# Performance work log

Measured on AMD Instinct MI355X. Metric: run time of the kernel, lower is better.

## Reference

```python
import jax, jax.numpy as jnp
import numpy as np

N_LEFT, N_RIGHT, E = 5000, 20000, 400000
HID, EDIM, NH, HD = 128, 4, 8, 16


def setup_inputs() -> dict:
    key = jax.random.key(0)
    ks = jax.random.split(key, 16)
    def lin(k, fi, fo):
        return jax.random.normal(k, (fi, fo), jnp.float32) / np.sqrt(fi)
    inp = {
        'left': jax.random.normal(ks[0], (N_LEFT, HID), jnp.float32),
        'right': jax.random.normal(ks[1], (N_RIGHT, HID), jnp.float32),
        'edge_features': jax.random.normal(ks[2], (E, EDIM), jnp.float32),
        'edge_src': jax.random.randint(ks[3], (E,), 0, N_LEFT, jnp.int32),
        'edge_dst': jax.random.randint(ks[4], (E,), 0, N_RIGHT, jnp.int32),
        'Wq': lin(ks[5], HID, HID),
        'Wk': lin(ks[6], HID, HID),
        'Wv': lin(ks[7], HID, HID),
        'Wke': lin(ks[8], EDIM, HID),
        'Wve': lin(ks[9], EDIM, HID),
        'Wout': lin(ks[10], HID, HID),
        'bn_gamma': jnp.ones((HID,), jnp.float32),
        'bn_beta': jnp.zeros((HID,), jnp.float32),
        'W1': lin(ks[11], 2 * HID, HID),
        'b1': jnp.zeros((HID,), jnp.float32),
        'W2': lin(ks[12], HID, HID),
        'b2': jnp.zeros((HID,), jnp.float32),
    }
    return inp


def _bipartite_attn(left, right, edge_features, edge_src, edge_dst,
                    Wq, Wk, Wv, Wke, Wve, Wout, bn_gamma, bn_beta, W1, b1, W2, b2):
    nr = right.shape[0]
    # project nodes once, then gather per edge (same math as gather-then-project)
    q = (right @ Wq).reshape(nr, NH, HD)[edge_dst]          # [E, H, D]
    k = (left @ Wk).reshape(-1, NH, HD)[edge_src]           # [E, H, D]
    v = (left @ Wv).reshape(-1, NH, HD)[edge_src]           # [E, H, D]
    ke = (edge_features @ Wke).reshape(-1, NH, HD)          # [E, H, D]
    ve = (edge_features @ Wve).reshape(-1, NH, HD)          # [E, H, D]
    logits = jnp.sum(q * (k + ke), axis=-1) / np.sqrt(HD)   # [E, H]
    # segment softmax over destination nodes (pyg_softmax)
    seg_max = jax.ops.segment_max(logits, edge_dst, num_segments=nr)  # [NR, H]
    seg_max = jnp.where(jnp.isfinite(seg_max), seg_max, 0.0)
    ex = jnp.exp(logits - seg_max[edge_dst])
    seg_sum = jax.ops.segment_sum(ex, edge_dst, num_segments=nr)      # [NR, H]
    alpha = ex / (seg_sum[edge_dst] + 1e-16)                          # [E, H]
    msg = (v + ve) * alpha[..., None]                                  # [E, H, D]
    agg = jax.ops.segment_sum(msg, edge_dst, num_segments=nr)         # [NR, H, D]
    out = agg.reshape(nr, NH * HD) @ Wout                              # [NR, HID]
    # BatchNorm1d (training-mode batch statistics, eps=1e-5)
    mean = jnp.mean(out, axis=0)
    var = jnp.var(out, axis=0)
    out = bn_gamma * (out - mean) * jax.lax.rsqrt(var + 1e-5) + bn_beta
    # output MLP on [out, right]
    h = jnp.concatenate([out, right], axis=-1) @ W1 + b1
    h = jax.nn.relu(h)
    return h @ W2 + b2


def reference(left, right, edge_features, edge_src, edge_dst,
              Wq, Wk, Wv, Wke, Wve, Wout, bn_gamma, bn_beta, W1, b1, W2, b2):
    return _bipartite_attn(left, right, edge_features, edge_src, edge_dst,
                           Wq, Wk, Wv, Wke, Wve, Wout, bn_gamma, bn_beta, W1, b1, W2, b2)
```

## Files before the change

kernel.cpp:

```cpp
#include <hip/hip_runtime.h>
#include <math.h>

#define N_LEFTC  5000
#define N_RIGHTC 20000
#define NEDGE    400000
#define MAXD     56

typedef __attribute__((ext_vector_type(8))) short bf16x8;
typedef __attribute__((ext_vector_type(4))) float f32x4;
typedef __attribute__((ext_vector_type(4))) unsigned short u16x4;
typedef __attribute__((ext_vector_type(8))) unsigned short u16x8;

__device__ __forceinline__ unsigned short f2bf(float x) {
    unsigned int u = __float_as_uint(x);
    u = (u + 0x7fffu + ((u >> 16) & 1u)) >> 16;
    return (unsigned short)u;
}
__device__ __forceinline__ float bf2f(unsigned short u) {
    return __uint_as_float(((unsigned int)u) << 16);
}

__device__ __forceinline__ bf16x8 loadA_f32(const float* p) {
    float4 f0 = *(const float4*)p;
    float4 f1 = *(const float4*)(p + 4);
    bf16x8 a;
    a[0] = (short)f2bf(f0.x); a[1] = (short)f2bf(f0.y);
    a[2] = (short)f2bf(f0.z); a[3] = (short)f2bf(f0.w);
    a[4] = (short)f2bf(f1.x); a[5] = (short)f2bf(f1.y);
    a[6] = (short)f2bf(f1.z); a[7] = (short)f2bf(f1.w);
    return a;
}

template<bool ABF, bool OBF>
__device__ __forceinline__ void gemm_body(const void* __restrict__ Av,
    const unsigned short* __restrict__ Bp, void* __restrict__ Cv, int M,
    int bid, int tid)
{
    const int l  = tid & 63;
    const int w  = tid >> 6;
    const int r0 = bid * 64 + w * 16;
    const int arow = r0 + (l & 15);
    const int kl = (l >> 4) * 8;
    f32x4 acc[8];
    #pragma unroll
    for (int ct = 0; ct < 8; ++ct) acc[ct] = (f32x4){0.f, 0.f, 0.f, 0.f};
    const bool aok = (arow < M);
    #pragma unroll
    for (int ks = 0; ks < 4; ++ks) {
        bf16x8 a = {0, 0, 0, 0, 0, 0, 0, 0};
        if (aok) {
            if (ABF) a = *(const bf16x8*)((const unsigned short*)Av + (size_t)arow * 128 + ks * 32 + kl);
            else     a = loadA_f32((const float*)Av + (size_t)arow * 128 + ks * 32 + kl);
        }
        #pragma unroll
        for (int ct = 0; ct < 8; ++ct) {
            bf16x8 b = *(const bf16x8*)(Bp + (((ks * 8 + ct) * 64 + l) << 3));
            acc[ct] = __builtin_amdgcn_mfma_f32_16x16x32_bf16(a, b, acc[ct], 0, 0, 0);
        }
    }
    const int orow = r0 + (l >> 4) * 4;
    const int oc   = l & 15;
    #pragma unroll
    for (int ct = 0; ct < 8; ++ct) {
        int col = ct * 16 + oc;
        #pragma unroll
        for (int r = 0; r < 4; ++r) {
            if (orow + r < M) {
                float v = acc[ct][r];
                if (OBF) ((unsigned short*)Cv)[(size_t)(orow + r) * 128 + col] = f2bf(v);
                else     ((float*)Cv)[(size_t)(orow + r) * 128 + col] = v;
            }
        }
    }
}

__global__ __launch_bounds__(256) void pack_init(const float* __restrict__ Wq,
    const float* __restrict__ Wk, const float* __restrict__ Wv,
    const float* __restrict__ Wout, const float* __restrict__ W2,
    const float* __restrict__ W1, unsigned short* __restrict__ Bp,
    int* __restrict__ cursors, float* __restrict__ stats)
{
    if (blockIdx.x < 448) {
        int i = blockIdx.x * 256 + threadIdx.x;
        const float* src; int rem;
        if (i < 81920) {
            int m = i >> 14; rem = i & 16383;
            src = (m == 0) ? Wq : (m == 1) ? Wk : (m == 2) ? Wv : (m == 3) ? Wout : W2;
        } else { rem = i - 81920; src = W1; }
        int j  = rem & 7;
        int l  = (rem >> 3) & 63;
        int ct = (rem >> 9) & 7;
        int ks = rem >> 12;
        int k  = ks * 32 + ((l >> 4) << 3) + j;
        int c  = (ct << 4) + (l & 15);
        Bp[i] = f2bf(src[k * 128 + c]);
    } else if (blockIdx.x < 527) {
        int i = (blockIdx.x - 448) * 256 + threadIdx.x;
        if (i < N_RIGHTC) cursors[i] = i * MAXD;
    } else {
        stats[threadIdx.x] = 0.f;
    }
}

__global__ __launch_bounds__(256) void scatter_qkv(const int* __restrict__ edst,
    const int* __restrict__ esrc, const float4* __restrict__ ef,
    int* __restrict__ cursors, float4* __restrict__ rec,
    const float* __restrict__ right, const float* __restrict__ left,
    const unsigned short* __restrict__ BpQ, const unsigned short* __restrict__ BpK,
    const unsigned short* __restrict__ BpV, unsigned short* __restrict__ Q,
    unsigned short* __restrict__ KV)
{
    if (blockIdx.x < 512) {
        for (int i = blockIdx.x * 256 + threadIdx.x; i < NEDGE; i += 512 * 256) {
            int d = edst[i];
            int p = atomicAdd(&cursors[d], 1);
            if (p < d * MAXD + MAXD) {
                rec[(size_t)p * 2] = ef[i];
                ((int*)rec)[(size_t)p * 8 + 4] = esrc[i];
            }
        }
    } else if (blockIdx.x < 825) {
        gemm_body<false, true>(right, BpQ, Q, N_RIGHTC, blockIdx.x - 512, threadIdx.x);
    } else {
        const int bid = blockIdx.x - 825;
        const int tid = threadIdx.x;
        const int l  = tid & 63;
        const int w  = tid >> 6;
        const int r0 = bid * 64 + w * 16;
        const int arow = r0 + (l & 15);
        const int kl = (l >> 4) * 8;
        f32x4 acck[8], accv[8];
        #pragma unroll
        for (int ct = 0; ct < 8; ++ct) { acck[ct] = (f32x4){0,0,0,0}; accv[ct] = (f32x4){0,0,0,0}; }
        const bool aok = (arow < N_LEFTC);
        #pragma unroll
        for (int ks = 0; ks < 4; ++ks) {
            bf16x8 a = {0, 0, 0, 0, 0, 0, 0, 0};
            if (aok) a = loadA_f32(left + (size_t)arow * 128 + ks * 32 + kl);
            #pragma unroll
            for (int ct = 0; ct < 8; ++ct) {
                int fo = ((ks * 8 + ct) * 64 + l) << 3;
                bf16x8 bk = *(const bf16x8*)(BpK + fo);
                bf16x8 bv = *(const bf16x8*)(BpV + fo);
                acck[ct] = __builtin_amdgcn_mfma_f32_16x16x32_bf16(a, bk, acck[ct], 0, 0, 0);
                accv[ct] = __builtin_amdgcn_mfma_f32_16x16x32_bf16(a, bv, accv[ct], 0, 0, 0);
            }
        }
        const int orow = r0 + (l >> 4) * 4;
        const int oc   = l & 15;
        #pragma unroll
        for (int ct = 0; ct < 8; ++ct) {
            int col = ct * 16 + oc;
            int cb  = ((col >> 2) << 3) + (col & 3);
            #pragma unroll
            for (int r = 0; r < 4; ++r) {
                if (orow + r < N_LEFTC) {
                    size_t base = (size_t)(orow + r) * 256 + cb;
                    KV[base]     = f2bf(acck[ct][r]);
                    KV[base + 4] = f2bf(accv[ct][r]);
                }
            }
        }
    }
}

__global__ __launch_bounds__(256) void attn_kernel(
    const unsigned short* __restrict__ qp, const unsigned short* __restrict__ kvp,
    const float4* __restrict__ rec, const int* __restrict__ cursors,
    const float* __restrict__ Wke, const float* __restrict__ Wve,
    unsigned short* __restrict__ agg)
{
    const int w    = threadIdx.x >> 6;
    const int l    = threadIdx.x & 63;
    const int half = l >> 5;
    const int hl   = l & 31;
    const int c0   = hl * 4;
    const int kvo  = hl * 8;
    const int gw   = blockIdx.x * 4 + w;
    const int nw   = gridDim.x * 4;

    float wke[4][4], wve[4][4];
    #pragma unroll
    for (int f = 0; f < 4; ++f) {
        float4 a = *(const float4*)(Wke + f * 128 + c0);
        wke[f][0] = a.x; wke[f][1] = a.y; wke[f][2] = a.z; wke[f][3] = a.w;
        float4 b = *(const float4*)(Wve + f * 128 + c0);
        wve[f][0] = b.x; wve[f][1] = b.y; wve[f][2] = b.z; wve[f][3] = b.w;
    }

    for (int d = gw; d < N_RIGHTC; d += nw) {
        u16x4 qu = *(const u16x4*)(qp + (size_t)d * 128 + c0);
        float qv[4] = { bf2f(qu[0]), bf2f(qu[1]), bf2f(qu[2]), bf2f(qu[3]) };

        float tq[4];
        #pragma unroll
        for (int f = 0; f < 4; ++f) {
            float tp = qv[0] * wke[f][0] + qv[1] * wke[f][1]
                     + qv[2] * wke[f][2] + qv[3] * wke[f][3];
            tp += __shfl_xor(tp, 1);
            tp += __shfl_xor(tp, 2);
            tq[f] = tp;
        }

        const int e0 = d * MAXD;
        int e1 = cursors[d];
        if (e1 > e0 + MAXD) e1 = e0 + MAXD;
        const int mid = (e0 + e1 + 1) >> 1;
        const int p0 = half ? mid : e0;
        const int pe = half ? e1 : mid;

        float s = 0.f;
        float av[4]  = {0.f, 0.f, 0.f, 0.f};
        float sef[4] = {0.f, 0.f, 0.f, 0.f};

        for (int p = p0; p < pe; p += 4) {
            int src_[4]; float4 ef_[4]; bool ok_[4];
            #pragma unroll
            for (int b = 0; b < 4; ++b) {
                int idx = p + b;
                ok_[b] = (idx < pe);
                int ii = ok_[b] ? idx : p0;
                ef_[b]  = rec[(size_t)ii * 2];
                src_[b] = ((const int*)rec)[(size_t)ii * 8 + 4];
            }
            u16x8 kv_[4];
            #pragma unroll
            for (int b = 0; b < 4; ++b)
                kv_[b] = *(const u16x8*)(kvp + (size_t)src_[b] * 256 + kvo);
            #pragma unroll
            for (int b = 0; b < 4; ++b) {
                float pp = qv[0] * bf2f(kv_[b][0]) + qv[1] * bf2f(kv_[b][1])
                         + qv[2] * bf2f(kv_[b][2]) + qv[3] * bf2f(kv_[b][3]);
                pp += __shfl_xor(pp, 1);
                pp += __shfl_xor(pp, 2);
                float4 f = ef_[b];
                float lg = (pp + f.x * tq[0] + f.y * tq[1] + f.z * tq[2] + f.w * tq[3]) * 0.25f;
                float e = ok_[b] ? __expf(lg) : 0.f;
                s += e;
                av[0] += e * bf2f(kv_[b][4]); av[1] += e * bf2f(kv_[b][5]);
                av[2] += e * bf2f(kv_[b][6]); av[3] += e * bf2f(kv_[b][7]);
                sef[0] += e * f.x; sef[1] += e * f.y; sef[2] += e * f.z; sef[3] += e * f.w;
            }
        }
        #pragma unroll
        for (int f = 0; f < 4; ++f) {
            av[0] += sef[f] * wve[f][0]; av[1] += sef[f] * wve[f][1];
            av[2] += sef[f] * wve[f][2]; av[3] += sef[f] * wve[f][3];
        }
        s += __shfl_xor(s, 32);
        #pragma unroll
        for (int j = 0; j < 4; ++j) av[j] += __shfl_xor(av[j], 32);
        if (half == 0) {
            float inv = 1.f / (s + 1e-16f);
            u16x4 o = { f2bf(av[0] * inv), f2bf(av[1] * inv),
                        f2bf(av[2] * inv), f2bf(av[3] * inv) };
            *(u16x4*)(agg + (size_t)d * 128 + c0) = o;
        }
    }
}

__global__ __launch_bounds__(256) void gemm_out0(const unsigned short* __restrict__ A,
    const unsigned short* __restrict__ Bp, unsigned short* __restrict__ C,
    float* __restrict__ stats, int M)
{
    __shared__ float sds[256];
    sds[threadIdx.x] = 0.f;
    __syncthreads();

    const int l  = threadIdx.x & 63;
    const int w  = threadIdx.x >> 6;
    const int r0 = blockIdx.x * 64 + w * 16;
    const int arow = r0 + (l & 15);
    const int kl = (l >> 4) * 8;
    f32x4 acc[8];
    #pragma unroll
    for (int ct = 0; ct < 8; ++ct) acc[ct] = (f32x4){0.f, 0.f, 0.f, 0.f};
    const bool aok = (arow < M);
    #pragma unroll
    for (int ks = 0; ks < 4; ++ks) {
        bf16x8 a = {0, 0, 0, 0, 0, 0, 0, 0};
        if (aok) a = *(const bf16x8*)(A + (size_t)arow * 128 + ks * 32 + kl);
        #pragma unroll
        for (int ct = 0; ct < 8; ++ct) {
            bf16x8 b = *(const bf16x8*)(Bp + (((ks * 8 + ct) * 64 + l) << 3));
            acc[ct] = __builtin_amdgcn_mfma_f32_16x16x32_bf16(a, b, acc[ct], 0, 0, 0);
        }
    }
    const int orow = r0 + (l >> 4) * 4;
    const int oc   = l & 15;
    #pragma unroll
    for (int ct = 0; ct < 8; ++ct) {
        int col = ct * 16 + oc;
        float cs = 0.f, cq = 0.f;
        #pragma unroll
        for (int r = 0; r < 4; ++r) {
            if (orow + r < M) {
                float v = acc[ct][r];
                C[(size_t)(orow + r) * 128 + col] = f2bf(v);
                cs += v; cq += v * v;
            }
        }
        atomicAdd(&sds[col], cs);
        atomicAdd(&sds[128 + col], cq);
    }
    __syncthreads();
    atomicAdd(&stats[threadIdx.x], sds[threadIdx.x]);
}

__global__ __launch_bounds__(256) void gemm_tail(const unsigned short* __restrict__ A1,
    const float* __restrict__ A2, const float* __restrict__ stats,
    const float* __restrict__ gamma, const float* __restrict__ beta,
    const unsigned short* __restrict__ Bp1, const float* __restrict__ b1,
    const unsigned short* __restrict__ Bp2, const float* __restrict__ b2,
    float* __restrict__ out, int M)
{
    __shared__ unsigned short h[64][136];
    __shared__ float sbn[256];
    if (threadIdx.x < 128) {
        int c = threadIdx.x;
        float mean = stats[c] * (1.f / N_RIGHTC);
        float var  = stats[128 + c] * (1.f / N_RIGHTC) - mean * mean;
        float sc   = gamma[c] * rsqrtf(var + 1e-5f);
        sbn[c]       = sc;
        sbn[128 + c] = beta[c] - mean * sc;
    }
    __syncthreads();

    const int l  = threadIdx.x & 63;
    const int w  = threadIdx.x >> 6;
    const int r0 = blockIdx.x * 64 + w * 16;
    const int arow = r0 + (l & 15);
    const int kl = (l >> 4) * 8;
    f32x4 acc[8];
    #pragma unroll
    for (int ct = 0; ct < 8; ++ct) acc[ct] = (f32x4){0.f, 0.f, 0.f, 0.f};
    const bool aok = (arow < M);
    #pragma unroll
    for (int ks = 0; ks < 8; ++ks) {
        bf16x8 a = {0, 0, 0, 0, 0, 0, 0, 0};
        if (aok) {
            if (ks < 4) {
                int k0 = ks * 32 + kl;
                bf16x8 raw = *(const bf16x8*)(A1 + (size_t)arow * 128 + k0);
                #pragma unroll
                for (int j = 0; j < 8; ++j)
                    a[j] = (short)f2bf(bf2f((unsigned short)raw[j]) * sbn[k0 + j] + sbn[128 + k0 + j]);
            } else {
                a = loadA_f32(A2 + (size_t)arow * 128 + (ks - 4) * 32 + kl);
            }
        }
        #pragma unroll
        for (int ct = 0; ct < 8; ++ct) {
            bf16x8 b = *(const bf16x8*)(Bp1 + (((ks * 8 + ct) * 64 + l) << 3));
            acc[ct] = __builtin_amdgcn_mfma_f32_16x16x32_bf16(a, b, acc[ct], 0, 0, 0);
        }
    }
    {
        const int lr0 = w * 16 + (l >> 4) * 4;
        const int oc  = l & 15;
        #pragma unroll
        for (int ct = 0; ct < 8; ++ct) {
            int col = ct * 16 + oc;
            float bv = b1[col];
            #pragma unroll
            for (int r = 0; r < 4; ++r)
                h[lr0 + r][col] = f2bf(fmaxf(acc[ct][r] + bv, 0.f));
        }
    }
    __syncthreads();
    #pragma unroll
    for (int ct = 0; ct < 8; ++ct) acc[ct] = (f32x4){0.f, 0.f, 0.f, 0.f};
    const int lrow = w * 16 + (l & 15);
    #pragma unroll
    for (int ks = 0; ks < 4; ++ks) {
        bf16x8 a = *(const bf16x8*)&h[lrow][ks * 32 + kl];
        #pragma unroll
        for (int ct = 0; ct < 8; ++ct) {
            bf16x8 b = *(const bf16x8*)(Bp2 + (((ks * 8 + ct) * 64 + l) << 3));
            acc[ct] = __builtin_amdgcn_mfma_f32_16x16x32_bf16(a, b, acc[ct], 0, 0, 0);
        }
    }
    const int orow = r0 + (l >> 4) * 4;
    const int oc   = l & 15;
    #pragma unroll
    for (int ct = 0; ct < 8; ++ct) {
        int col = ct * 16 + oc;
        float bv = b2[col];
        #pragma unroll
        for (int r = 0; r < 4; ++r)
            if (orow + r < M)
                out[(size_t)(orow + r) * 128 + col] = acc[ct][r] + bv;
    }
}

extern "C" void kernel_launch(void* const* d_in, const int* in_sizes, int n_in,
                              void* d_out, int out_size, void* d_ws, size_t ws_size,
                              hipStream_t stream)
{
    const float* left  = (const float*)d_in[0];
    const float* right = (const float*)d_in[1];
    const float* ef    = (const float*)d_in[2];
    const int*   esrc  = (const int*)d_in[3];
    const int*   edst  = (const int*)d_in[4];
    const float* Wq    = (const float*)d_in[5];
    const float* Wk    = (const float*)d_in[6];
    const float* Wv    = (const float*)d_in[7];
    const float* Wke   = (const float*)d_in[8];
    const float* Wve   = (const float*)d_in[9];
    const float* Wout  = (const float*)d_in[10];
    const float* gamma = (const float*)d_in[11];
    const float* beta  = (const float*)d_in[12];
    const float* W1    = (const float*)d_in[13];
    const float* b1    = (const float*)d_in[14];
    const float* W2    = (const float*)d_in[15];
    const float* b2    = (const float*)d_in[16];
    float* out = (float*)d_out;

    char* ws = (char*)d_ws;
    float* stats   = (float*)(ws + 0);
    int*   cursors = (int*)  (ws + 1024);
    unsigned short* Bp     = (unsigned short*)(ws + 81024);
    unsigned short* qproj  = (unsigned short*)(ws + 310400);
    unsigned short* kvproj = (unsigned short*)(ws + 5430400);
    unsigned short* agg    = (unsigned short*)(ws + 7990400);
    float4* rec    = (float4*)(ws + 13110400);
    unsigned short* out0   = (unsigned short*)(ws + 13110400);

    pack_init<<<528, 256, 0, stream>>>(Wq, Wk, Wv, Wout, W2, W1, Bp, cursors, stats);

    scatter_qkv<<<904, 256, 0, stream>>>(edst, esrc, (const float4*)ef, cursors, rec,
                                         right, left, Bp, Bp + 16384, Bp + 32768,
                                         qproj, kvproj);

    attn_kernel<<<2048, 256, 0, stream>>>(qproj, kvproj, rec, cursors, Wke, Wve, agg);

    gemm_out0<<<(N_RIGHTC + 63) / 64, 256, 0, stream>>>(agg, Bp + 49152, out0, stats, N_RIGHTC);

    gemm_tail<<<(N_RIGHTC + 63) / 64, 256, 0, stream>>>(out0, right, stats, gamma, beta,
                                                        Bp + 81920, b1, Bp + 65536, b2,
                                                        out, N_RIGHTC);
}
```

Measured before the change: 116.9 us.

## Fuse output GEMM and MLP tail via grid barrier; pack edge records

Merges the Wout GEMM with BatchNorm statistics and the MLP tail into one kernel. A software grid-wide barrier (an atomic counter spin-wait) lets every block see the complete batch statistics before the tail runs, which removes one kernel launch. Edge records shrink from 32 to 16 bytes by storing the edge features as bf16 next to the source index, cutting scatter and attention memory traffic. The barrier assumes all 313 blocks are co-resident, and the bf16 edge features lose some precision.

Result: slower. 163.5 us (+39.8%).

```diff
diff --git a/kernel.cpp b/kernel.cpp
--- a/kernel.cpp
+++ b/kernel.cpp
@@ -78,7 +78,7 @@
     const float* __restrict__ Wk, const float* __restrict__ Wv,
     const float* __restrict__ Wout, const float* __restrict__ W2,
     const float* __restrict__ W1, unsigned short* __restrict__ Bp,
-    int* __restrict__ cursors, float* __restrict__ stats)
+    int* __restrict__ cursors, float* __restrict__ stats, int* __restrict__ done)
 {
     if (blockIdx.x < 448) {
         int i = blockIdx.x * 256 + threadIdx.x;
@@ -99,12 +99,13 @@
         if (i < N_RIGHTC) cursors[i] = i * MAXD;
     } else {
         stats[threadIdx.x] = 0.f;
+        if (threadIdx.x == 0) *done = 0;
     }
 }
 
 __global__ __launch_bounds__(256) void scatter_qkv(const int* __restrict__ edst,
     const int* __restrict__ esrc, const float4* __restrict__ ef,
-    int* __restrict__ cursors, float4* __restrict__ rec,
+    int* __restrict__ cursors, uint4* __restrict__ rec,
     const float* __restrict__ right, const float* __restrict__ left,
     const unsigned short* __restrict__ BpQ, const unsigned short* __restrict__ BpK,
     const unsigned short* __restrict__ BpV, unsigned short* __restrict__ Q,
@@ -115,8 +116,13 @@
             int d = edst[i];
             int p = atomicAdd(&cursors[d], 1);
             if (p < d * MAXD + MAXD) {
-                rec[(size_t)p * 2] = ef[i];
-                ((int*)rec)[(size_t)p * 8 + 4] = esrc[i];
+                float4 e = ef[i];
+                uint4 r;
+                r.x = (unsigned)f2bf(e.x) | ((unsigned)f2bf(e.y) << 16);
+                r.y = (unsigned)f2bf(e.z) | ((unsigned)f2bf(e.w) << 16);
+                r.z = (unsigned)esrc[i];
+                r.w = 0u;
+                rec[p] = r;
             }
         }
     } else if (blockIdx.x < 825) {
@@ -166,7 +172,7 @@
 
 __global__ __launch_bounds__(256) void attn_kernel(
     const unsigned short* __restrict__ qp, const unsigned short* __restrict__ kvp,
-    const float4* __restrict__ rec, const int* __restrict__ cursors,
+    const uint4* __restrict__ rec, const int* __restrict__ cursors,
     const float* __restrict__ Wke, const float* __restrict__ Wve,
     unsigned short* __restrict__ agg)
 {
@@ -220,8 +226,12 @@
                 int idx = p + b;
                 ok_[b] = (idx < pe);
                 int ii = ok_[b] ? idx : p0;
-                ef_[b]  = rec[(size_t)ii * 2];
-                src_[b] = ((const int*)rec)[(size_t)ii * 8 + 4];
+                uint4 r = rec[ii];
+                ef_[b] = make_float4(bf2f((unsigned short)(r.x & 0xffffu)),
+                                     bf2f((unsigned short)(r.x >> 16)),
+                                     bf2f((unsigned short)(r.y & 0xffffu)),
+                                     bf2f((unsigned short)(r.y >> 16)));
+                src_[b] = (int)r.z;
             }
             u16x8 kv_[4];
             #pragma unroll
@@ -259,65 +269,76 @@
     }
 }
 
-__global__ __launch_bounds__(256) void gemm_out0(const unsigned short* __restrict__ A,
-    const unsigned short* __restrict__ Bp, unsigned short* __restrict__ C,
-    float* __restrict__ stats, int M)
-{
-    __shared__ float sds[256];
-    sds[threadIdx.x] = 0.f;
-    __syncthreads();
-
-    const int l  = threadIdx.x & 63;
-    const int w  = threadIdx.x >> 6;
+__global__ __launch_bounds__(256) void gemm_fused(const unsigned short* __restrict__ agg,
+    const unsigned short* __restrict__ BpO, unsigned short* __restrict__ out0,
+    float* __restrict__ stats, int* __restrict__ done,
+    const float* __restrict__ right, const float* __restrict__ gamma,
+    const float* __restrict__ beta,
+    const unsigned short* __restrict__ Bp1, const float* __restrict__ b1,
+    const unsigned short* __restrict__ Bp2, const float* __restrict__ b2,
+    float* __restrict__ out)
+{
+    const int M = N_RIGHTC;
+    const int tid = threadIdx.x;
+    const int l  = tid & 63;
+    const int w  = tid >> 6;
     const int r0 = blockIdx.x * 64 + w * 16;
     const int arow = r0 + (l & 15);
     const int kl = (l >> 4) * 8;
+    const bool aok = (arow < M);
+
+    __shared__ float sds[256];
+    __shared__ unsigned short h[64][136];
+    __shared__ float sbn[256];
+
+    sds[tid] = 0.f;
+    __syncthreads();
     f32x4 acc[8];
     #pragma unroll
     for (int ct = 0; ct < 8; ++ct) acc[ct] = (f32x4){0.f, 0.f, 0.f, 0.f};
-    const bool aok = (arow < M);
     #pragma unroll
     for (int ks = 0; ks < 4; ++ks) {
         bf16x8 a = {0, 0, 0, 0, 0, 0, 0, 0};
-        if (aok) a = *(const bf16x8*)(A + (size_t)arow * 128 + ks * 32 + kl);
-        #pragma unroll
-        for (int ct = 0; ct < 8; ++ct) {
-            bf16x8 b = *(const bf16x8*)(Bp + (((ks * 8 + ct) * 64 + l) << 3));
+        if (aok) a = *(const bf16x8*)(agg + (size_t)arow * 128 + ks * 32 + kl);
+        #pragma unroll
+        for (int ct = 0; ct < 8; ++ct) {
+            bf16x8 b = *(const bf16x8*)(BpO + (((ks * 8 + ct) * 64 + l) << 3));
             acc[ct] = __builtin_amdgcn_mfma_f32_16x16x32_bf16(a, b, acc[ct], 0, 0, 0);
         }
     }
-    const int orow = r0 + (l >> 4) * 4;
-    const int oc   = l & 15;
-    #pragma unroll
-    for (int ct = 0; ct < 8; ++ct) {
-        int col = ct * 16 + oc;
-        float cs = 0.f, cq = 0.f;
-        #pragma unroll
-        for (int r = 0; r < 4; ++r) {
-            if (orow + r < M) {
-                float v = acc[ct][r];
-                C[(size_t)(orow + r) * 128 + col] = f2bf(v);
-                cs += v; cq += v * v;
-            }
-        }
-        atomicAdd(&sds[col], cs);
-        atomicAdd(&sds[128 + col], cq);
-    }
-    __syncthreads();
-    atomicAdd(&stats[threadIdx.x], sds[threadIdx.x]);
-}
-
-__global__ __launch_bounds__(256) void gemm_tail(const unsigned short* __restrict__ A1,
-    const float* __restrict__ A2, const float* __restrict__ stats,
-    const float* __restrict__ gamma, const float* __restrict__ beta,
-    const unsigned short* __restrict__ Bp1, const float* __restrict__ b1,
-    const unsigned short* __restrict__ Bp2, const float* __restrict__ b2,
-    float* __restrict__ out, int M)
-{
-    __shared__ unsigned short h[64][136];
-    __shared__ float sbn[256];
-    if (threadIdx.x < 128) {
-        int c = threadIdx.x;
+    {
+        const int orow = r0 + (l >> 4) * 4;
+        const int oc   = l & 15;
+        #pragma unroll
+        for (int ct = 0; ct < 8; ++ct) {
+            int col = ct * 16 + oc;
+            float cs = 0.f, cq = 0.f;
+            #pragma unroll
+            for (int r = 0; r < 4; ++r) {
+                if (orow + r < M) {
+                    float v = acc[ct][r];
+                    out0[(size_t)(orow + r) * 128 + col] = f2bf(v);
+                    cs += v; cq += v * v;
+                }
+            }
+            atomicAdd(&sds[col], cs);
+            atomicAdd(&sds[128 + col], cq);
+        }
+    }
+    __syncthreads();
+    atomicAdd(&stats[tid], sds[tid]);
+
+    __threadfence();
+    __syncthreads();
+    if (tid == 0) {
+        atomicAdd(done, 1);
+        while (atomicAdd(done, 0) < (int)gridDim.x) {}
+    }
+    __syncthreads();
+    __threadfence();
+
+    if (tid < 128) {
+        int c = tid;
         float mean = stats[c] * (1.f / N_RIGHTC);
         float var  = stats[128 + c] * (1.f / N_RIGHTC) - mean * mean;
         float sc   = gamma[c] * rsqrtf(var + 1e-5f);
@@ -326,27 +347,20 @@
     }
     __syncthreads();
 
-    const int l  = threadIdx.x & 63;
-    const int w  = threadIdx.x >> 6;
-    const int r0 = blockIdx.x * 64 + w * 16;
-    const int arow = r0 + (l & 15);
-    const int kl = (l >> 4) * 8;
-    f32x4 acc[8];
     #pragma unroll
     for (int ct = 0; ct < 8; ++ct) acc[ct] = (f32x4){0.f, 0.f, 0.f, 0.f};
-    const bool aok = (arow < M);
     #pragma unroll
     for (int ks = 0; ks < 8; ++ks) {
         bf16x8 a = {0, 0, 0, 0, 0, 0, 0, 0};
         if (aok) {
             if (ks < 4) {
                 int k0 = ks * 32 + kl;
-                bf16x8 raw = *(const bf16x8*)(A1 + (size_t)arow * 128 + k0);
+                bf16x8 raw = *(const bf16x8*)(out0 + (size_t)arow * 128 + k0);
                 #pragma unroll
                 for (int j = 0; j < 8; ++j)
                     a[j] = (short)f2bf(bf2f((unsigned short)raw[j]) * sbn[k0 + j] + sbn[128 + k0 + j]);
             } else {
-                a = loadA_f32(A2 + (size_t)arow * 128 + (ks - 4) * 32 + kl);
+                a = loadA_f32(right + (size_t)arow * 128 + (ks - 4) * 32 + kl);
             }
         }
         #pragma unroll
@@ -380,16 +394,18 @@
             acc[ct] = __builtin_amdgcn_mfma_f32_16x16x32_bf16(a, b, acc[ct], 0, 0, 0);
         }
     }
-    const int orow = r0 + (l >> 4) * 4;
-    const int oc   = l & 15;
-    #pragma unroll
-    for (int ct = 0; ct < 8; ++ct) {
-        int col = ct * 16 + oc;
-        float bv = b2[col];
-        #pragma unroll
-        for (int r = 0; r < 4; ++r)
-            if (orow + r < M)
-                out[(size_t)(orow + r) * 128 + col] = acc[ct][r] + bv;
+    {
+        const int orow = r0 + (l >> 4) * 4;
+        const int oc   = l & 15;
+        #pragma unroll
+        for (int ct = 0; ct < 8; ++ct) {
+            int col = ct * 16 + oc;
+            float bv = b2[col];
+            #pragma unroll
+            for (int r = 0; r < 4; ++r)
+                if (orow + r < M)
+                    out[(size_t)(orow + r) * 128 + col] = acc[ct][r] + bv;
+        }
     }
 }
 
@@ -418,15 +434,16 @@
 
     char* ws = (char*)d_ws;
     float* stats   = (float*)(ws + 0);
-    int*   cursors = (int*)  (ws + 1024);
-    unsigned short* Bp     = (unsigned short*)(ws + 81024);
-    unsigned short* qproj  = (unsigned short*)(ws + 310400);
-    unsigned short* kvproj = (unsigned short*)(ws + 5430400);
-    unsigned short* agg    = (unsigned short*)(ws + 7990400);
-    float4* rec    = (float4*)(ws + 13110400);
-    unsigned short* out0   = (unsigned short*)(ws + 13110400);
-
-    pack_init<<<528, 256, 0, stream>>>(Wq, Wk, Wv, Wout, W2, W1, Bp, cursors, stats);
+    int*   done    = (int*)  (ws + 1024);
+    int*   cursors = (int*)  (ws + 1152);
+    unsigned short* Bp     = (unsigned short*)(ws + 81152);
+    unsigned short* qproj  = (unsigned short*)(ws + 310528);
+    unsigned short* kvproj = (unsigned short*)(ws + 5430528);
+    unsigned short* agg    = (unsigned short*)(ws + 7990528);
+    uint4* rec     = (uint4*)(ws + 13110528);
+    unsigned short* out0   = (unsigned short*)(ws + 13110528);
+
+    pack_init<<<528, 256, 0, stream>>>(Wq, Wk, Wv, Wout, W2, W1, Bp, cursors, stats, done);
 
     scatter_qkv<<<904, 256, 0, stream>>>(edst, esrc, (const float4*)ef, cursors, rec,
                                          right, left, Bp, Bp + 16384, Bp + 32768,
@@ -434,9 +451,7 @@
 
     attn_kernel<<<2048, 256, 0, stream>>>(qproj, kvproj, rec, cursors, Wke, Wve, agg);
 
-    gemm_out0<<<(N_RIGHTC + 63) / 64, 256, 0, stream>>>(agg, Bp + 49152, out0, stats, N_RIGHTC);
-
-    gemm_tail<<<(N_RIGHTC + 63) / 64, 256, 0, stream>>>(out0, right, stats, gamma, beta,
-                                                        Bp + 81920, b1, Bp + 65536, b2,
-                                                        out, N_RIGHTC);
-}
+    gemm_fused<<<313, 256, 0, stream>>>(agg, Bp + 49152, out0, stats, done,
+                                        right, gamma, beta,
+                                        Bp + 81920, b1, Bp + 65536, b2, out);
+}
```
